# Performance work log

Measured on AMD Instinct MI355X. Metric: run time of the kernel, lower is better.

Reference implementation:

```python
import jax, jax.numpy as jnp
import numpy as np

WS = (7, 7, 7)          # (Wz, Wh, Ww)
NUM_HEADS = 3


def rel_position_index(ws):
    # Faithful to meshgrid_3d in the source: arrays are reversed, grid i varies
    # along axis i, so coords are stacked in (w, h, z) order.
    wz, wh, ww = ws
    g = np.meshgrid(np.arange(ww), np.arange(wh), np.arange(wz), indexing='ij')
    coords = np.stack(g)                      # (3, ww, wh, wz)
    flat = coords.reshape(3, -1)              # (3, N)
    rel = flat[:, :, None] - flat[:, None, :]  # (3, N, N)
    rel = rel.transpose(1, 2, 0).astype(np.int64)  # (N, N, 3)
    rel[:, :, 0] += wz - 1
    rel[:, :, 1] += wh - 1
    rel[:, :, 2] += ww - 1
    rel[:, :, 0] *= (2 * wh - 1) * (2 * ww - 1)
    rel[:, :, 1] *= (2 * ww - 1)
    return rel.sum(-1)                        # (N, N) in [0, (2W-1)^3)


REL_IDX = jnp.asarray(rel_position_index(WS).reshape(-1), dtype=jnp.int32)


def setup_inputs() -> dict:
    key = jax.random.key(0)
    ks = jax.random.split(key, 6)
    B, N, C = 256, 343, 96
    nW = 32
    x = jax.random.normal(ks[0], (B, N, C), dtype=jnp.float32)
    # shifted-window mask: 0 where attendable, -100 where blocked
    keep = jax.random.uniform(ks[1], (nW, N, N)) < 0.9
    mask = jnp.where(keep, 0.0, -100.0).astype(jnp.float32)
    w_qkv = jax.random.normal(ks[2], (C, 3 * C), dtype=jnp.float32) * 0.05
    b_qkv = jnp.zeros((3 * C,), jnp.float32)
    bias_table = jax.random.normal(ks[3], (2197, NUM_HEADS), dtype=jnp.float32) * 0.02
    w_proj = jax.random.normal(ks[4], (C, C), dtype=jnp.float32) * 0.05
    b_proj = jnp.zeros((C,), jnp.float32)
    return {"x": x, "mask": mask, "w_qkv": w_qkv, "b_qkv": b_qkv,
            "bias_table": bias_table, "w_proj": w_proj, "b_proj": b_proj}


def reference(x, mask, w_qkv, b_qkv, bias_table, w_proj, b_proj):
    B, N, C = x.shape
    H = NUM_HEADS
    hd = C // H
    scale = hd ** -0.5  # qk_scale is None -> head_dim**-0.5 (swin v1 path)
    # QKV projection, split to heads: (3, B, H, N, hd)
    qkv = (x @ w_qkv + b_qkv).reshape(B, N, 3, H, hd).transpose(2, 0, 3, 1, 4)
    q, k, v = qkv[0] * scale, qkv[1], qkv[2]
    attn = jnp.einsum('bhnd,bhmd->bhnm', q, k)        # (B, H, N, N)
    # gathered relative-position bias -> (H, N, N)
    bias = bias_table[REL_IDX].reshape(N, N, H).transpose(2, 0, 1)
    attn = attn + bias[None]
    # shifted-window mask add: reshape to (B//nW, nW, H, N, N)
    nW = mask.shape[0]
    attn = attn.reshape(B // nW, nW, H, N, N) + mask[None, :, None]
    attn = jax.nn.softmax(attn.reshape(B, H, N, N), axis=-1)
    out = jnp.einsum('bhnm,bhmd->bhnd', attn, v)      # (B, H, N, hd)
    out = out.transpose(0, 2, 1, 3).reshape(B, N, C)
    return out @ w_proj + b_proj
```

## Files before the change

kernel.cpp:

```cpp
#include <hip/hip_runtime.h>

#define N_TOK 343
#define NP 352
#define C_DIM 96
#define HEADS 3
#define HD 32
#define B_SZ 256
#define NW 32
#define QKV_COLS 288
#define NKT 11

#define QKV_ELEMS (B_SZ * HEADS * N_TOK * HD)
#define X2_ELEMS ((long)B_SZ * N_TOK * C_DIM)
#define CMB_ELEMS ((long)NW * HEADS * N_TOK * NP)
#define WT_PITCH 104

typedef _Float16 f16;
typedef _Float16 f16x2 __attribute__((ext_vector_type(2)));
typedef _Float16 f16x4 __attribute__((ext_vector_type(4)));
typedef _Float16 f16x8 __attribute__((ext_vector_type(8)));
typedef float f32x4 __attribute__((ext_vector_type(4)));

__global__ __launch_bounds__(256) void wprep_kernel(
    const float* __restrict__ w_qkv, const float* __restrict__ w_proj,
    f16* __restrict__ wt_qkv, f16* __restrict__ wt_proj) {
  const int e = blockIdx.x * 256 + threadIdx.x;
  if (e < QKV_COLS * 96) {
    const int cc = e / 96, k = e % 96;
    wt_qkv[e] = (f16)w_qkv[k * QKV_COLS + cc];
  } else {
    const int e2 = e - QKV_COLS * 96;
    if (e2 < 96 * 96) {
      const int cc = e2 / 96, k = e2 % 96;
      wt_proj[e2] = (f16)w_proj[k * 96 + cc];
    }
  }
}

__global__ __launch_bounds__(384) void cmb_kernel(
    const float* __restrict__ mask, const float* __restrict__ bias_table,
    f16* __restrict__ cmb) {
  const int q = blockIdx.x;
  const int w = blockIdx.y;
  const int key = threadIdx.x;
  if (key >= NP) return;
  const int bn = (q / 49) * 169 + ((q / 7) % 7) * 13 + (q % 7);
  const float LOG2E = 1.4426950408889634f;
  float mv = 0.f;
  int idx = 0;
  const bool valid = (key < N_TOK);
  if (valid) {
    const int bm = (key / 49) * 169 + ((key / 7) % 7) * 13 + (key % 7);
    idx = (bn - bm + 1098) * HEADS;
    mv = mask[((long)w * N_TOK + q) * N_TOK + key];
  }
#pragma unroll
  for (int h = 0; h < HEADS; ++h) {
    const float val = valid ? (bias_table[idx + h] + mv) * LOG2E : -14427.0f;
    cmb[((long)(w * HEADS + h) * N_TOK + q) * NP + key] = (f16)val;
  }
}

__global__ __launch_bounds__(512) void qkv_mfma_kernel(
    const float* __restrict__ x, const f16* __restrict__ wt,
    const float* __restrict__ bias,
    f16* __restrict__ Q, f16* __restrict__ K, f16* __restrict__ V) {
  __shared__ f16 wtL[QKV_COLS][WT_PITCH];
  __shared__ f16 sh[8][16][40];
  const int tid = threadIdx.x;
  const int wave = tid >> 6, lane = tid & 63;
  const int c = lane & 15, g = lane >> 4;
  const long rowTile = (long)blockIdx.x * 128 + wave * 16;
  const long arow = rowTile + c;

  for (int u = tid; u < QKV_COLS * 12; u += 512) {
    const int r = u / 12, ch = u % 12;
    *(f16x8*)&wtL[r][ch * 8] = *(const f16x8*)(wt + r * 96 + ch * 8);
  }

  f16x8 af[3];
#pragma unroll
  for (int ks = 0; ks < 3; ++ks) {
    const float* px = x + arow * 96 + ks * 32 + g * 8;
    const float4 lo = *(const float4*)px;
    const float4 hi = *(const float4*)(px + 4);
    f16x8 v;
    v[0] = (f16)lo.x; v[1] = (f16)lo.y; v[2] = (f16)lo.z; v[3] = (f16)lo.w;
    v[4] = (f16)hi.x; v[5] = (f16)hi.y; v[6] = (f16)hi.z; v[7] = (f16)hi.w;
    af[ks] = v;
  }
  __syncthreads();

  const int rowL = (int)rowTile + (lane >> 2);
  const int bL = rowL / N_TOK, nL = rowL % N_TOK;

  const f32x4 zero = {0.f, 0.f, 0.f, 0.f};
  const float scale = 0.17677669529663687f * 1.4426950408889634f;

#pragma unroll
  for (int p = 0; p < 9; ++p) {
    const int which = p / 3;
    const int h = p % 3;
    const float mult = (which == 0) ? scale : 1.0f;
#pragma unroll
    for (int e = 0; e < 2; ++e) {
      const int ct = 2 * p + e;
      f32x4 acc = zero;
#pragma unroll
      for (int ks = 0; ks < 3; ++ks) {
        const f16x8 bf = *(const f16x8*)&wtL[ct * 16 + c][ks * 32 + g * 8];
        acc = __builtin_amdgcn_mfma_f32_16x16x32_f16(af[ks], bf, acc, 0, 0, 0);
      }
      const float bv = bias[ct * 16 + c];
#pragma unroll
      for (int r = 0; r < 4; ++r)
        sh[wave][4 * g + r][(e << 4) + c] = (f16)((acc[r] + bv) * mult);
    }
    __builtin_amdgcn_wave_barrier();
    const f16x8 po = *(const f16x8*)&sh[wave][lane >> 2][(lane & 3) * 8];
    __builtin_amdgcn_wave_barrier();
    f16* dst = (which == 0) ? Q : (which == 1) ? K : V;
    *(f16x8*)(dst + (((long)bL * HEADS + h) * N_TOK + nL) * HD + (lane & 3) * 8) = po;
  }
}

__global__ __launch_bounds__(256) void attn_kernel(
    const f16* __restrict__ Qh, const f16* __restrict__ Kh,
    const f16* __restrict__ Vh, const f16* __restrict__ CMB,
    f16* __restrict__ X2h) {
  __shared__ f16 Ks[NP][40];
  __shared__ f16 Vt[HD][356];

  const int blk = blockIdx.x;
  const int b = blk / HEADS;
  const int h = blk % HEADS;
  const int tid = threadIdx.x;
  const int wave = tid >> 6;
  const int lane = tid & 63;
  const int c = lane & 15;
  const int g = lane >> 4;

  const f16* Kg = Kh + (long)blk * (N_TOK * HD);
  const f16* Vg = Vh + (long)blk * (N_TOK * HD);
  const f16* Qg = Qh + (long)blk * (N_TOK * HD);

  for (int u = tid; u < NP * 4; u += 256) {
    const int key = u >> 2, j = u & 3;
    f16x8 val = {0, 0, 0, 0, 0, 0, 0, 0};
    if (key < N_TOK) val = *(const f16x8*)(Kg + key * HD + j * 8);
    *(f16x8*)&Ks[key][j * 8] = val;
  }
  for (int i = tid; i < N_TOK * 16; i += 256) {
    const int n = i >> 4, dp = i & 15;
    const f16x2 v2 = *(const f16x2*)(Vg + n * HD + dp * 2);
    Vt[2 * dp][n] = v2.x;
    Vt[2 * dp + 1][n] = v2.y;
  }
  for (int i = tid; i < HD * 13; i += 256) Vt[i / 13][N_TOK + i % 13] = (f16)0;
  __syncthreads();

  const int w = b & (NW - 1);
  const f32x4 zero = {0.f, 0.f, 0.f, 0.f};

  for (int qt = wave; qt < NP / 16; qt += 4) {
    const int q = qt * 16 + c;
    const int qrow = (q < N_TOK) ? q : (N_TOK - 1);
    const f16* cmrow = CMB + ((long)(w * HEADS + h) * N_TOK + qrow) * NP;

    f16x4 cmA[NKT], cmB[NKT];
#pragma unroll
    for (int kt = 0; kt < NKT; ++kt) {
      cmA[kt] = *(const f16x4*)(cmrow + 32 * kt + 4 * g);
      cmB[kt] = *(const f16x4*)(cmrow + 32 * kt + 16 + 4 * g);
    }
    const f16x8 qf = *(const f16x8*)(Qg + qrow * HD + g * 8);

    f32x4 acc0 = zero, acc1 = zero;
    float lsum = 0.f;

#pragma unroll
    for (int kt = 0; kt < NKT; ++kt) {
      const f16x8 kf0 = *(const f16x8*)&Ks[32 * kt + c][g * 8];
      const f16x8 kf1 = *(const f16x8*)&Ks[32 * kt + 16 + c][g * 8];

      const f32x4 s0 = __builtin_amdgcn_mfma_f32_16x16x32_f16(kf0, qf, zero, 0, 0, 0);
      const f32x4 s1 = __builtin_amdgcn_mfma_f32_16x16x32_f16(kf1, qf, zero, 0, 0, 0);

      float p0[4], p1[4];
#pragma unroll
      for (int r = 0; r < 4; ++r) {
        p0[r] = __builtin_amdgcn_exp2f(s0[r] + (float)cmA[kt][r]);
        p1[r] = __builtin_amdgcn_exp2f(s1[r] + (float)cmB[kt][r]);
        lsum += p0[r] + p1[r];
      }
      const f16x2 a0 = __builtin_bit_cast(f16x2, __builtin_amdgcn_cvt_pkrtz(p0[0], p0[1]));
      const f16x2 a1 = __builtin_bit_cast(f16x2, __builtin_amdgcn_cvt_pkrtz(p0[2], p0[3]));
      const f16x2 a2 = __builtin_bit_cast(f16x2, __builtin_amdgcn_cvt_pkrtz(p1[0], p1[1]));
      const f16x2 a3 = __builtin_bit_cast(f16x2, __builtin_amdgcn_cvt_pkrtz(p1[2], p1[3]));
      const f16x4 plo = __builtin_shufflevector(a0, a1, 0, 1, 2, 3);
      const f16x4 phi = __builtin_shufflevector(a2, a3, 0, 1, 2, 3);
      const f16x8 pf = __builtin_shufflevector(plo, phi, 0, 1, 2, 3, 4, 5, 6, 7);

      const f16x4 va0 = *(const f16x4*)&Vt[c][32 * kt + 4 * g];
      const f16x4 va1 = *(const f16x4*)&Vt[c][32 * kt + 16 + 4 * g];
      const f16x4 vb0 = *(const f16x4*)&Vt[16 + c][32 * kt + 4 * g];
      const f16x4 vb1 = *(const f16x4*)&Vt[16 + c][32 * kt + 16 + 4 * g];
      const f16x8 vf0 = __builtin_shufflevector(va0, va1, 0, 1, 2, 3, 4, 5, 6, 7);
      const f16x8 vf1 = __builtin_shufflevector(vb0, vb1, 0, 1, 2, 3, 4, 5, 6, 7);

      acc0 = __builtin_amdgcn_mfma_f32_16x16x32_f16(vf0, pf, acc0, 0, 0, 0);
      acc1 = __builtin_amdgcn_mfma_f32_16x16x32_f16(vf1, pf, acc1, 0, 0, 0);
    }

    lsum += __shfl_xor(lsum, 16);
    lsum += __shfl_xor(lsum, 32);
    const float inv = 1.f / lsum;

    if (q < N_TOK) {
      f16* orow = X2h + ((long)b * N_TOK + q) * C_DIM + h * HD;
      f16x4 o0, o1;
#pragma unroll
      for (int r = 0; r < 4; ++r) {
        o0[r] = (f16)(acc0[r] * inv);
        o1[r] = (f16)(acc1[r] * inv);
      }
      *(f16x4*)(orow + 4 * g) = o0;
      *(f16x4*)(orow + 16 + 4 * g) = o1;
    }
  }
}

__global__ __launch_bounds__(256) void proj_mfma_kernel(
    const f16* __restrict__ X2h, const f16* __restrict__ wt,
    const float* __restrict__ bias, float* __restrict__ out) {
  __shared__ f16 wtL[C_DIM][WT_PITCH];
  __shared__ float shp[4][16][100];
  const int tid = threadIdx.x;
  const int wave = tid >> 6, lane = tid & 63;
  const int c = lane & 15, g = lane >> 4;
  const long rowTile = (long)blockIdx.x * 64 + wave * 16;
  const long arow = rowTile + c;

  for (int u = tid; u < C_DIM * 12; u += 256) {
    const int r = u / 12, ch = u % 12;
    *(f16x8*)&wtL[r][ch * 8] = *(const f16x8*)(wt + r * 96 + ch * 8);
  }

  f16x8 af[3];
#pragma unroll
  for (int ks = 0; ks < 3; ++ks)
    af[ks] = *(const f16x8*)(X2h + arow * 96 + ks * 32 + g * 8);
  __syncthreads();

  const f32x4 zero = {0.f, 0.f, 0.f, 0.f};
#pragma unroll
  for (int ct = 0; ct < 6; ++ct) {
    f32x4 acc = zero;
#pragma unroll
    for (int ks = 0; ks < 3; ++ks) {
      const f16x8 bf = *(const f16x8*)&wtL[ct * 16 + c][ks * 32 + g * 8];
      acc = __builtin_amdgcn_mfma_f32_16x16x32_f16(af[ks], bf, acc, 0, 0, 0);
    }
    const float bv = bias[ct * 16 + c];
#pragma unroll
    for (int r = 0; r < 4; ++r)
      shp[wave][4 * g + r][ct * 16 + c] = acc[r] + bv;
  }
  __builtin_amdgcn_wave_barrier();
#pragma unroll
  for (int i = 0; i < 6; ++i) {
    const int u = lane + 64 * i;
    const int row = u / 24, ch = u % 24;
    const float4 v = *(const float4*)&shp[wave][row][ch * 4];
    *(float4*)(out + (rowTile + row) * 96 + ch * 4) = v;
  }
}

extern "C" void kernel_launch(void* const* d_in, const int* in_sizes, int n_in,
                              void* d_out, int out_size, void* d_ws, size_t ws_size,
                              hipStream_t stream) {
  const float* x          = (const float*)d_in[0];
  const float* mask       = (const float*)d_in[1];
  const float* w_qkv      = (const float*)d_in[2];
  const float* b_qkv      = (const float*)d_in[3];
  const float* bias_table = (const float*)d_in[4];
  const float* w_proj     = (const float*)d_in[5];
  const float* b_proj     = (const float*)d_in[6];
  float* out = (float*)d_out;

  f16* Qh = (f16*)d_ws;
  f16* Kh = Qh + QKV_ELEMS;
  f16* Vh = Kh + QKV_ELEMS;
  f16* X2h = Vh + QKV_ELEMS;
  f16* CMB = X2h + X2_ELEMS;
  f16* WTQ = CMB + CMB_ELEMS;
  f16* WTP = WTQ + QKV_COLS * 96;

  const int wBlocks = (QKV_COLS * 96 + 96 * 96 + 255) / 256;
  const int qkvBlocks = (B_SZ * N_TOK) / 128;
  const int projBlocks = (B_SZ * N_TOK) / 64;

  wprep_kernel<<<wBlocks, 256, 0, stream>>>(w_qkv, w_proj, WTQ, WTP);
  cmb_kernel<<<dim3(N_TOK, NW), 384, 0, stream>>>(mask, bias_table, CMB);
  qkv_mfma_kernel<<<qkvBlocks, 512, 0, stream>>>(x, WTQ, b_qkv, Qh, Kh, Vh);
  attn_kernel<<<B_SZ * HEADS, 256, 0, stream>>>(Qh, Kh, Vh, CMB, X2h);
  proj_mfma_kernel<<<projBlocks, 256, 0, stream>>>(X2h, WTP, b_proj, out);
}
```

Baseline: 200.2 us.

## Pre-transpose V in separate kernel and widen attention blocks to 512 threads

Adds a vtr_kernel that transposes each head's V into a padded global [HD][NP] layout, so attention blocks can load Vt with vector copies instead of scattered 2-byte LDS writes. The attention kernel moves from 256 to 512 threads (8 waves sharing the same K/V tile), and mask+bias rows are now loaded per key tile inside a non-unrolled loop instead of being fully prefetched into registers. The aim is cheaper staging and better latency hiding. The cost is an extra kernel launch, an extra global round trip for V, and possibly more exposed load latency now that the loop is no longer unrolled.

```diff
diff --git a/kernel.cpp b/kernel.cpp
--- a/kernel.cpp
+++ b/kernel.cpp
@@ -13,6 +13,7 @@
 #define QKV_ELEMS (B_SZ * HEADS * N_TOK * HD)
 #define X2_ELEMS ((long)B_SZ * N_TOK * C_DIM)
 #define CMB_ELEMS ((long)NW * HEADS * N_TOK * NP)
+#define VTG_ELEMS ((long)B_SZ * HEADS * HD * NP)
 #define WT_PITCH 104
 
 typedef _Float16 f16;
@@ -124,9 +125,42 @@
   }
 }
 
-__global__ __launch_bounds__(256) void attn_kernel(
+__global__ __launch_bounds__(256) void vtr_kernel(
+    const f16* __restrict__ V, f16* __restrict__ VtG) {
+  __shared__ f16 t[64][40];
+  const int blk = blockIdx.x;
+  const f16* src = V + (long)blk * (N_TOK * HD);
+  f16* dst = VtG + (long)blk * (HD * NP);
+  const int tid = threadIdx.x;
+
+  for (int c0 = 0; c0 < NP; c0 += 64) {
+    {
+      const int row = tid >> 2;
+      const int n = c0 + row;
+      const int ch = (tid & 3) * 8;
+      f16x8 v = {0, 0, 0, 0, 0, 0, 0, 0};
+      if (n < N_TOK) v = *(const f16x8*)(src + n * HD + ch);
+      *(f16x8*)&t[row][ch] = v;
+    }
+    __syncthreads();
+    {
+      const int d = tid >> 3;
+      const int nch = tid & 7;
+      const int n0 = c0 + nch * 8;
+      if (n0 < NP) {
+        f16x8 o;
+#pragma unroll
+        for (int j = 0; j < 8; ++j) o[j] = t[nch * 8 + j][d];
+        *(f16x8*)(dst + d * NP + n0) = o;
+      }
+    }
+    __syncthreads();
+  }
+}
+
+__global__ __launch_bounds__(512) void attn_kernel(
     const f16* __restrict__ Qh, const f16* __restrict__ Kh,
-    const f16* __restrict__ Vh, const f16* __restrict__ CMB,
+    const f16* __restrict__ VtG, const f16* __restrict__ CMB,
     f16* __restrict__ X2h) {
   __shared__ f16 Ks[NP][40];
   __shared__ f16 Vt[HD][356];
@@ -141,47 +175,38 @@
   const int g = lane >> 4;
 
   const f16* Kg = Kh + (long)blk * (N_TOK * HD);
-  const f16* Vg = Vh + (long)blk * (N_TOK * HD);
+  const f16* Vg = VtG + (long)blk * (HD * NP);
   const f16* Qg = Qh + (long)blk * (N_TOK * HD);
 
-  for (int u = tid; u < NP * 4; u += 256) {
+  for (int u = tid; u < NP * 4; u += 512) {
     const int key = u >> 2, j = u & 3;
     f16x8 val = {0, 0, 0, 0, 0, 0, 0, 0};
     if (key < N_TOK) val = *(const f16x8*)(Kg + key * HD + j * 8);
     *(f16x8*)&Ks[key][j * 8] = val;
   }
-  for (int i = tid; i < N_TOK * 16; i += 256) {
-    const int n = i >> 4, dp = i & 15;
-    const f16x2 v2 = *(const f16x2*)(Vg + n * HD + dp * 2);
-    Vt[2 * dp][n] = v2.x;
-    Vt[2 * dp + 1][n] = v2.y;
-  }
-  for (int i = tid; i < HD * 13; i += 256) Vt[i / 13][N_TOK + i % 13] = (f16)0;
+  for (int u = tid; u < HD * 44; u += 512) {
+    const int d = u / 44, ch = (u % 44) * 8;
+    *(f16x8*)&Vt[d][ch] = *(const f16x8*)(Vg + d * NP + ch);
+  }
   __syncthreads();
 
   const int w = b & (NW - 1);
   const f32x4 zero = {0.f, 0.f, 0.f, 0.f};
 
-  for (int qt = wave; qt < NP / 16; qt += 4) {
+  for (int qt = wave; qt < NP / 16; qt += 8) {
     const int q = qt * 16 + c;
     const int qrow = (q < N_TOK) ? q : (N_TOK - 1);
+    const f16x8 qf = *(const f16x8*)(Qg + qrow * HD + g * 8);
     const f16* cmrow = CMB + ((long)(w * HEADS + h) * N_TOK + qrow) * NP;
-
-    f16x4 cmA[NKT], cmB[NKT];
-#pragma unroll
-    for (int kt = 0; kt < NKT; ++kt) {
-      cmA[kt] = *(const f16x4*)(cmrow + 32 * kt + 4 * g);
-      cmB[kt] = *(const f16x4*)(cmrow + 32 * kt + 16 + 4 * g);
-    }
-    const f16x8 qf = *(const f16x8*)(Qg + qrow * HD + g * 8);
 
     f32x4 acc0 = zero, acc1 = zero;
     float lsum = 0.f;
 
-#pragma unroll
     for (int kt = 0; kt < NKT; ++kt) {
       const f16x8 kf0 = *(const f16x8*)&Ks[32 * kt + c][g * 8];
       const f16x8 kf1 = *(const f16x8*)&Ks[32 * kt + 16 + c][g * 8];
+      const f16x4 cm0 = *(const f16x4*)(cmrow + 32 * kt + 4 * g);
+      const f16x4 cm1 = *(const f16x4*)(cmrow + 32 * kt + 16 + 4 * g);
 
       const f32x4 s0 = __builtin_amdgcn_mfma_f32_16x16x32_f16(kf0, qf, zero, 0, 0, 0);
       const f32x4 s1 = __builtin_amdgcn_mfma_f32_16x16x32_f16(kf1, qf, zero, 0, 0, 0);
@@ -189,8 +214,8 @@
       float p0[4], p1[4];
 #pragma unroll
       for (int r = 0; r < 4; ++r) {
-        p0[r] = __builtin_amdgcn_exp2f(s0[r] + (float)cmA[kt][r]);
-        p1[r] = __builtin_amdgcn_exp2f(s1[r] + (float)cmB[kt][r]);
+        p0[r] = __builtin_amdgcn_exp2f(s0[r] + (float)cm0[r]);
+        p1[r] = __builtin_amdgcn_exp2f(s1[r] + (float)cm1[r]);
         lsum += p0[r] + p1[r];
       }
       const f16x2 a0 = __builtin_bit_cast(f16x2, __builtin_amdgcn_cvt_pkrtz(p0[0], p0[1]));
@@ -295,6 +320,7 @@
   f16* CMB = X2h + X2_ELEMS;
   f16* WTQ = CMB + CMB_ELEMS;
   f16* WTP = WTQ + QKV_COLS * 96;
+  f16* VtG = WTP + 96 * 96;
 
   const int wBlocks = (QKV_COLS * 96 + 96 * 96 + 255) / 256;
   const int qkvBlocks = (B_SZ * N_TOK) / 128;
@@ -303,6 +329,7 @@
   wprep_kernel<<<wBlocks, 256, 0, stream>>>(w_qkv, w_proj, WTQ, WTP);
   cmb_kernel<<<dim3(N_TOK, NW), 384, 0, stream>>>(mask, bias_table, CMB);
   qkv_mfma_kernel<<<qkvBlocks, 512, 0, stream>>>(x, WTQ, b_qkv, Qh, Kh, Vh);
-  attn_kernel<<<B_SZ * HEADS, 256, 0, stream>>>(Qh, Kh, Vh, CMB, X2h);
+  vtr_kernel<<<B_SZ * HEADS, 256, 0, stream>>>(Vh, VtG);
+  attn_kernel<<<B_SZ * HEADS, 512, 0, stream>>>(Qh, Kh, VtG, CMB, X2h);
   proj_mfma_kernel<<<projBlocks, 256, 0, stream>>>(X2h, WTP, b_proj, out);
 }
```

After: 187.0 us. 1.07x faster.
